# Optimization experiments

Hardware: AMD Instinct MI355X
Metric: run time of the kernel (lower is better)

## Reference

```python
import jax, jax.numpy as jnp
import numpy as np

B, N, DIM = 1, 65536, 256
H, D, G = 8, 64, 64  # heads, dim_head, slice_num


def setup_inputs() -> dict:
    key = jax.random.key(0)
    ks = jax.random.split(key, 16)
    s = 0.02
    return {
        "x": jax.random.normal(ks[0], (B, N, DIM), jnp.float32),
        "Wx": jax.random.normal(ks[1], (H * D, DIM), jnp.float32) * s,
        "bx": jnp.zeros((H * D,), jnp.float32),
        "Wt1": jax.random.normal(ks[2], (G, D), jnp.float32) * s,
        "bt1": jnp.zeros((G,), jnp.float32),
        "Wt2": jax.random.normal(ks[3], (1, G), jnp.float32) * s,
        "bt2": jnp.zeros((1,), jnp.float32),
        "bias": jnp.ones((1, H, 1, 1), jnp.float32) * 0.5,
        "Ws": jax.random.normal(ks[4], (G, D), jnp.float32) * s,
        "bs": jnp.zeros((G,), jnp.float32),
        "Wq": jax.random.normal(ks[5], (D, D), jnp.float32) * s,
        "Wk": jax.random.normal(ks[6], (D, D), jnp.float32) * s,
        "Wv": jax.random.normal(ks[7], (D, D), jnp.float32) * s,
        "Wout": jax.random.normal(ks[8], (DIM, H * D), jnp.float32) * s,
        "bout": jnp.zeros((DIM,), jnp.float32),
        "u": jax.random.uniform(ks[9], (B, H, N, G), jnp.float32),
    }


def _gelu(t):
    return jax.nn.gelu(t, approximate=False)  # torch default exact GELU


def reference(x, Wx, bx, Wt1, bt1, Wt2, bt2, bias, Ws, bs, Wq, Wk, Wv, Wout, bout, u):
    b, n, _ = x.shape
    h, d, g = Wt1.shape[1] and bias.shape[1], Wq.shape[0], Ws.shape[0]
    # project and split heads: b n (h d) -> b h n d
    x_mid = (x @ Wx.T + bx).reshape(b, n, h, d).transpose(0, 2, 1, 3)
    # per-point temperature MLP + learned bias, clamped
    temp = _gelu(_gelu(x_mid @ Wt1.T + bt1) @ Wt2.T + bt2) + bias  # (b,h,n,1)
    temp = jnp.maximum(temp, 0.01)
    # gumbel-softmax slice routing (soft, hard=False)
    logits = x_mid @ Ws.T + bs  # (b,h,n,g)
    gnoise = -jnp.log(-jnp.log(u + 1e-8) + 1e-8)
    slice_weights = jax.nn.softmax((logits + gnoise) / temp, axis=-1)
    norm = slice_weights.sum(axis=2)  # (b,h,g)
    # gather-aggregate points into g slice tokens
    slice_tokens = jnp.einsum('bhnc,bhng->bhgc', x_mid, slice_weights)
    slice_tokens = slice_tokens / (norm[..., None] + 1e-5)
    # tiny g x g attention among slice tokens
    q = slice_tokens @ Wq.T
    k = slice_tokens @ Wk.T
    v = slice_tokens @ Wv.T
    attn = jax.nn.softmax((q @ k.transpose(0, 1, 3, 2)) * (d ** -0.5), axis=-1)
    out_slice = attn @ v  # (b,h,g,d)
    # scatter-combine back to points
    out = jnp.einsum('bhgd,bhng->bhnd', out_slice, slice_weights)
    out = out.transpose(0, 2, 1, 3).reshape(b, n, h * d)
    return out @ Wout.T + bout
```

## Files before the change

### kernel.cpp

```cpp
#include <hip/hip_runtime.h>
#include <math.h>

#define NPTS  65536
#define DIMX  256
#define NH    8
#define HDIM  512

typedef __attribute__((ext_vector_type(4))) float f32x4;
typedef __attribute__((ext_vector_type(8))) short short8;
typedef __attribute__((ext_vector_type(8))) unsigned short ushort8;
typedef __attribute__((ext_vector_type(4))) unsigned short us4;

__device__ __forceinline__ ushort f2bf(float f) {
    unsigned x = __float_as_uint(f);
    return (ushort)((x + 0x7fffu + ((x >> 16) & 1u)) >> 16);
}
__device__ __forceinline__ float bf2f(ushort u) {
    return __uint_as_float((unsigned)u << 16);
}
__device__ __forceinline__ float erf_fast(float x) {
    float ax = fabsf(x);
    float t  = __builtin_amdgcn_rcpf(1.0f + 0.3275911f * ax);
    float p  = fmaf(fmaf(fmaf(fmaf(1.061405429f, t, -1.453152027f), t,
                   1.421413741f), t, -0.284496736f), t, 0.254829592f) * t;
    float y  = 1.0f - p * __expf(-ax * ax);
    return copysignf(y, x);
}
__device__ __forceinline__ float gelu_fast(float x) {
    return 0.5f * x * (1.0f + erf_fast(x * 0.7071067811865476f));
}

__global__ __launch_bounds__(256)
void prep_kernel(const float* __restrict__ x, const float* __restrict__ Wx,
                 const float* __restrict__ Ws, const float* __restrict__ Wt1,
                 ushort* __restrict__ xb, ushort* __restrict__ Wxb,
                 ushort* __restrict__ wb) {
    const int t = threadIdx.x;
    const int b = blockIdx.x;
    if (b < 8192) {
        size_t idx = (size_t)b * 2048 + t * 8;
        float4 a0 = *(const float4*)&x[idx];
        float4 a1 = *(const float4*)&x[idx + 4];
        ushort8 v = { f2bf(a0.x), f2bf(a0.y), f2bf(a0.z), f2bf(a0.w),
                      f2bf(a1.x), f2bf(a1.y), f2bf(a1.z), f2bf(a1.w) };
        *(ushort8*)&xb[idx] = v;
    } else if (b < 8256) {
        int idx = (b - 8192) * 2048 + t * 8;
        float4 a0 = *(const float4*)&Wx[idx];
        float4 a1 = *(const float4*)&Wx[idx + 4];
        ushort8 v = { f2bf(a0.x), f2bf(a0.y), f2bf(a0.z), f2bf(a0.w),
                      f2bf(a1.x), f2bf(a1.y), f2bf(a1.z), f2bf(a1.w) };
        *(ushort8*)&Wxb[idx] = v;
    } else {
        int idx = (b - 8256) * 2048 + t * 8;
        int row = idx >> 6, col = idx & 63;
        const float* src = (row < 64) ? &Ws[row * 64 + col]
                                      : &Wt1[(row - 64) * 64 + col];
        float4 a0 = *(const float4*)src;
        float4 a1 = *(const float4*)(src + 4);
        ushort8 v = { f2bf(a0.x), f2bf(a0.y), f2bf(a0.z), f2bf(a0.w),
                      f2bf(a1.x), f2bf(a1.y), f2bf(a1.z), f2bf(a1.w) };
        *(ushort8*)&wb[idx] = v;
    }
}

__global__ __launch_bounds__(256)
void xmid_lgt1_kernel(const ushort* __restrict__ A, const ushort* __restrict__ B,
                      const float* __restrict__ bias,
                      const ushort* __restrict__ wb,
                      const float* __restrict__ bs,  const float* __restrict__ bt1,
                      const float* __restrict__ Wt2, const float* __restrict__ bt2,
                      const float* __restrict__ biasp,
                      const float* __restrict__ u,
                      ushort* __restrict__ xmb, ushort* __restrict__ swb) {
    __shared__ __align__(16) ushort pool[2][128][64];
    const int hp = blockIdx.y;
    const int m0 = blockIdx.x * 128, n0 = hp * 128;
    const int t = threadIdx.x, l = t & 63, w = t >> 6;
    const int wr = w >> 1, wc = w & 1;
    const int lr = l & 15, lq = l >> 4;
    const float LOG2E = 1.4426950408889634f;
    const float LN2   = 0.6931471805599453f;
    const float SH2   = 36.0673760222f;

    f32x4 acc[4][4];
    #pragma unroll
    for (int mi = 0; mi < 4; ++mi)
        #pragma unroll
        for (int ni = 0; ni < 4; ++ni) acc[mi][ni] = (f32x4){0.f, 0.f, 0.f, 0.f};

    for (int ks = 0; ks < 4; ++ks) {
        __syncthreads();
        #pragma unroll
        for (int i = 0; i < 4; ++i) {
            int idx = i * 256 + t;
            int row = idx >> 3, g = idx & 7;
            ushort8 av = *(const ushort8*)&A[(size_t)(m0 + row) * 256 + ks * 64 + g * 8];
            *(ushort8*)&pool[0][row][(g ^ (row & 7)) * 8] = av;
            ushort8 bv = *(const ushort8*)&B[(size_t)(n0 + row) * 256 + ks * 64 + g * 8];
            *(ushort8*)&pool[1][row][(g ^ (row & 7)) * 8] = bv;
        }
        __syncthreads();
        #pragma unroll
        for (int kf = 0; kf < 2; ++kf) {
            short8 af[4], bfr[4];
            #pragma unroll
            for (int mi = 0; mi < 4; ++mi) {
                int row = wr * 64 + mi * 16 + lr, g = kf * 4 + lq;
                af[mi] = *(const short8*)&pool[0][row][(g ^ (row & 7)) * 8];
            }
            #pragma unroll
            for (int ni = 0; ni < 4; ++ni) {
                int row = wc * 64 + ni * 16 + lr, g = kf * 4 + lq;
                bfr[ni] = *(const short8*)&pool[1][row][(g ^ (row & 7)) * 8];
            }
            #pragma unroll
            for (int mi = 0; mi < 4; ++mi)
                #pragma unroll
                for (int ni = 0; ni < 4; ++ni)
                    acc[mi][ni] = __builtin_amdgcn_mfma_f32_16x16x32_bf16(
                        af[mi], bfr[ni], acc[mi][ni], 0, 0, 0);
        }
    }

    __syncthreads();
    ushort (* __restrict__ Xl)[128] = (ushort (*)[128])(&pool[0][0][0]);
    #pragma unroll
    for (int ni = 0; ni < 4; ++ni) {
        int colL = wc * 64 + ni * 16 + lr;
        float bb = bias[n0 + colL];
        int gg = colL >> 3, c7 = colL & 7;
        #pragma unroll
        for (int mi = 0; mi < 4; ++mi)
            #pragma unroll
            for (int j = 0; j < 4; ++j) {
                int row = wr * 64 + mi * 16 + lq * 4 + j;
                Xl[row][(gg ^ (row & 7)) * 8 + c7] = f2bf(acc[mi][ni][j] + bb);
            }
    }
    __syncthreads();
    #pragma unroll
    for (int i = 0; i < 8; ++i) {
        int e = i * 256 + t;
        int row = e >> 4, gg = e & 15;
        ushort8 v = *(const ushort8*)&Xl[row][(gg ^ (row & 7)) * 8];
        *(ushort8*)&xmb[(size_t)(m0 + row) * 512 + n0 + gg * 8] = v;
    }

    const float bt2v = bt2[0];
    float bsr[4], bt1r[4], wt2r[4];
    #pragma unroll
    for (int ni = 0; ni < 4; ++ni) {
        bsr[ni]  = bs [ni * 16 + lr];
        bt1r[ni] = bt1[ni * 16 + lr];
        wt2r[ni] = Wt2[ni * 16 + lr];
    }

    #pragma unroll
    for (int hh = 0; hh < 2; ++hh) {
        const int h = hp * 2 + hh;
        const float biasph = biasp[h];

        f32x4 acc2[2][8];
        #pragma unroll
        for (int mi = 0; mi < 2; ++mi)
            #pragma unroll
            for (int ni = 0; ni < 8; ++ni) acc2[mi][ni] = (f32x4){0.f, 0.f, 0.f, 0.f};

        #pragma unroll
        for (int kf = 0; kf < 2; ++kf) {
            const int g = kf * 4 + lq;
            short8 af[2], bfr[8];
            #pragma unroll
            for (int mi = 0; mi < 2; ++mi) {
                int row = w * 32 + mi * 16 + lr;
                int gg = hh * 8 + g;
                af[mi] = *(const short8*)&Xl[row][(gg ^ (row & 7)) * 8];
            }
            #pragma unroll
            for (int ni = 0; ni < 8; ++ni)
                bfr[ni] = *(const short8*)&wb[(size_t)(ni * 16 + lr) * 64 + g * 8];
            #pragma unroll
            for (int mi = 0; mi < 2; ++mi)
                #pragma unroll
                for (int ni = 0; ni < 8; ++ni)
                    acc2[mi][ni] = __builtin_amdgcn_mfma_f32_16x16x32_bf16(
                        af[mi], bfr[ni], acc2[mi][ni], 0, 0, 0);
        }

        #pragma unroll
        for (int mi = 0; mi < 2; ++mi) {
            float uu[4][4];
            #pragma unroll
            for (int jj = 0; jj < 4; ++jj) {
                const int n = m0 + w * 32 + mi * 16 + lq * 4 + jj;
                const float* up = &u[((size_t)h * NPTS + n) * 64 + lr];
                #pragma unroll
                for (int ni = 0; ni < 4; ++ni) uu[jj][ni] = up[ni * 16];
            }
            float ts[4];
            #pragma unroll
            for (int jj = 0; jj < 4; ++jj) {
                float s = 0.f;
                #pragma unroll
                for (int ni = 0; ni < 4; ++ni)
                    s += gelu_fast(acc2[mi][ni + 4][jj] + bt1r[ni]) * wt2r[ni];
                ts[jj] = s;
            }
            #pragma unroll
            for (int off = 1; off <= 8; off <<= 1) {
                #pragma unroll
                for (int jj = 0; jj < 4; ++jj) ts[jj] += __shfl_xor(ts[jj], off);
            }
            float invt[4], invt2[4];
            #pragma unroll
            for (int jj = 0; jj < 4; ++jj) {
                float tmp = gelu_fast(ts[jj] + bt2v) + biasph;
                tmp = fmaxf(tmp, 0.01f);
                invt[jj]  = __builtin_amdgcn_rcpf(tmp);
                invt2[jj] = invt[jj] * LOG2E;
            }
            float sv[4][4], ps[4] = {0.f, 0.f, 0.f, 0.f};
            #pragma unroll
            for (int jj = 0; jj < 4; ++jj) {
                #pragma unroll
                for (int ni = 0; ni < 4; ++ni) {
                    float L1 = __log2f(uu[jj][ni] + 1e-8f);
                    float inner = fmaf(-LN2, L1, 1e-8f);
                    float L2v = __log2f(inner);
                    float base = fmaf(acc2[mi][ni][jj] + bsr[ni], invt2[jj], -SH2);
                    sv[jj][ni] = __builtin_amdgcn_exp2f(fmaf(-invt[jj], L2v, base));
                    ps[jj] += sv[jj][ni];
                }
            }
            #pragma unroll
            for (int off = 1; off <= 8; off <<= 1) {
                #pragma unroll
                for (int jj = 0; jj < 4; ++jj) ps[jj] += __shfl_xor(ps[jj], off);
            }
            #pragma unroll
            for (int jj = 0; jj < 4; ++jj) {
                const int n = m0 + w * 32 + mi * 16 + lq * 4 + jj;
                const float inv = __builtin_amdgcn_rcpf(ps[jj]);
                ushort* sp = &swb[(size_t)n * 512 + h * 64 + lr];
                #pragma unroll
                for (int ni = 0; ni < 4; ++ni)
                    sp[ni * 16] = f2bf(sv[jj][ni] * inv);
            }
        }
    }
}

__global__ __launch_bounds__(256)
void gather_mfma_kernel(const ushort* __restrict__ xmb, const ushort* __restrict__ swb,
                        float* __restrict__ stp, float* __restrict__ normp) {
    __shared__ __align__(16) ushort tile[2][64][128];
    ushort (* __restrict__ swT)[128] = tile[0];
    ushort (* __restrict__ xT )[128] = tile[1];
    const int h  = blockIdx.y;
    const int n0 = blockIdx.x * 1024;
    const int t  = threadIdx.x, l = t & 63, w = t >> 6;
    const int lr = l & 15, lq = l >> 4;
    const int gb = t & 7;
    const int ng = t >> 3;

    f32x4 acc[4][4];
    #pragma unroll
    for (int gi = 0; gi < 4; ++gi)
        #pragma unroll
        for (int ci = 0; ci < 4; ++ci) acc[gi][ci] = (f32x4){0.f, 0.f, 0.f, 0.f};
    float nrm8[8];
    #pragma unroll
    for (int j = 0; j < 8; ++j) nrm8[j] = 0.f;

    for (int r = 0; r < 8; ++r) {
        const int nt = n0 + r * 128;
        ushort8 sv[4], xv[4];
        #pragma unroll
        for (int i = 0; i < 4; ++i) {
            int n = nt + ng * 4 + i;
            sv[i] = *(const ushort8*)&swb[(size_t)n * 512 + h * 64 + gb * 8];
            xv[i] = *(const ushort8*)&xmb[(size_t)n * 512 + h * 64 + gb * 8];
        }
        __syncthreads();
        #pragma unroll
        for (int j = 0; j < 8; ++j) {
            int g   = gb * 8 + j;
            int swz = (ng >> 1) ^ (g & 7) ^ ((g >> 3) & 7);
            int off = swz * 8 + (ng & 1) * 4;
            us4 s4 = { sv[0][j], sv[1][j], sv[2][j], sv[3][j] };
            us4 x4 = { xv[0][j], xv[1][j], xv[2][j], xv[3][j] };
            *(us4*)&swT[g][off] = s4;
            *(us4*)&xT [g][off] = x4;
            nrm8[j] += (bf2f(sv[0][j]) + bf2f(sv[1][j]))
                     + (bf2f(sv[2][j]) + bf2f(sv[3][j]));
        }
        __syncthreads();
        short8 af[4], bfr[4];
        #pragma unroll
        for (int gi = 0; gi < 4; ++gi) {
            int g   = gi * 16 + lr;
            int swz = (w * 4 + lq) ^ (g & 7) ^ ((g >> 3) & 7);
            af[gi]  = *(const short8*)&swT[g][swz * 8];
            bfr[gi] = *(const short8*)&xT [g][swz * 8];
        }
        #pragma unroll
        for (int gi = 0; gi < 4; ++gi)
            #pragma unroll
            for (int ci = 0; ci < 4; ++ci)
                acc[gi][ci] = __builtin_amdgcn_mfma_f32_16x16x32_bf16(
                    af[gi], bfr[ci], acc[gi][ci], 0, 0, 0);
    }

    float* sred = (float*)tile;
    const size_t stbase = ((size_t)h * 64 + blockIdx.x) * 4096;
    #pragma unroll
    for (int half = 0; half < 2; ++half) {
        __syncthreads();
        #pragma unroll
        for (int gg = 0; gg < 2; ++gg) {
            int gi = half * 2 + gg;
            #pragma unroll
            for (int ci = 0; ci < 4; ++ci)
                #pragma unroll
                for (int j = 0; j < 4; ++j)
                    sred[(w * 32 + gg * 16 + lq * 4 + j) * 64 + ci * 16 + lr]
                        = acc[gi][ci][j];
        }
        __syncthreads();
        #pragma unroll
        for (int i = 0; i < 8; ++i) {
            int e = i * 256 + t;
            float s = (sred[e] + sred[2048 + e]) + (sred[4096 + e] + sred[6144 + e]);
            stp[stbase + half * 2048 + e] = s;
        }
    }

    __syncthreads();
    float* narr = (float*)tile;
    #pragma unroll
    for (int j = 0; j < 8; ++j) narr[ng * 64 + gb * 8 + j] = nrm8[j];
    __syncthreads();
    if (t < 64) {
        float s = 0.f;
        #pragma unroll 8
        for (int k = 0; k < 32; ++k) s += narr[k * 64 + t];
        normp[((size_t)h * 64 + blockIdx.x) * 64 + t] = s;
    }
}

__global__ __launch_bounds__(256)
void reduce_st_kernel(const float* __restrict__ stp, const float* __restrict__ normp,
                      float* __restrict__ st_red, float* __restrict__ nrm) {
    const int h = blockIdx.x;
    const int e = blockIdx.y * 256 + threadIdx.x;
    float s = 0.f;
    #pragma unroll 8
    for (int ch = 0; ch < 64; ++ch)
        s += stp[((size_t)h * 64 + ch) * 4096 + e];
    st_red[(size_t)h * 4096 + e] = s;
    if (blockIdx.y == 0 && threadIdx.x < 64) {
        float ns = 0.f;
        #pragma unroll 8
        for (int ch = 0; ch < 64; ++ch)
            ns += normp[((size_t)h * 64 + ch) * 64 + threadIdx.x];
        nrm[h * 64 + threadIdx.x] = ns + 1e-5f;
    }
}

__global__ __launch_bounds__(256)
void attn_small_kernel(const float* __restrict__ st_red, const float* __restrict__ nrm,
                       const float* __restrict__ Wq, const float* __restrict__ Wk,
                       const float* __restrict__ Wv, float* __restrict__ osl) {
    __shared__ float st[64][68];
    __shared__ float ql[64][68];
    __shared__ float kl[64][68];
    __shared__ float vl[64][68];
    __shared__ float sc[64][68];
    __shared__ float nl[64];
    const int h = blockIdx.x;
    const int t = threadIdx.x;

    if (t < 64) nl[t] = nrm[h * 64 + t];
    __syncthreads();
    for (int e = t; e < 4096; e += 256)
        st[e>>6][e&63] = st_red[(size_t)h * 4096 + e] / nl[e>>6];
    __syncthreads();
    for (int e = t; e < 4096; e += 256) {
        int g = e >> 6, dd = e & 63;
        float aq = 0.f, ak = 0.f, av = 0.f;
        for (int cc = 0; cc < 64; ++cc) {
            float sv = st[g][cc];
            aq = fmaf(sv, Wq[dd*64 + cc], aq);
            ak = fmaf(sv, Wk[dd*64 + cc], ak);
            av = fmaf(sv, Wv[dd*64 + cc], av);
        }
        ql[g][dd] = aq; kl[g][dd] = ak; vl[g][dd] = av;
    }
    __syncthreads();
    for (int e = t; e < 4096; e += 256) {
        int g = e >> 6, gp = e & 63;
        float s = 0.f;
        for (int dd = 0; dd < 64; ++dd) s = fmaf(ql[g][dd], kl[gp][dd], s);
        sc[g][gp] = s * 0.125f;
    }
    __syncthreads();
    if (t < 64) {
        float m = -1e30f;
        for (int j = 0; j < 64; ++j) m = fmaxf(m, sc[t][j]);
        float ssum = 0.f;
        for (int j = 0; j < 64; ++j) { float p = expf(sc[t][j] - m); sc[t][j] = p; ssum += p; }
        float inv = 1.f / ssum;
        for (int j = 0; j < 64; ++j) sc[t][j] *= inv;
    }
    __syncthreads();
    for (int e = t; e < 4096; e += 256) {
        int g = e >> 6, dd = e & 63;
        float s = 0.f;
        for (int gp = 0; gp < 64; ++gp) s = fmaf(sc[g][gp], vl[gp][dd], s);
        osl[(size_t)h * 4096 + e] = s;
    }
}

__global__ __launch_bounds__(256)
void fold_kernel(const float* __restrict__ osl, const float* __restrict__ Wout,
                 ushort* __restrict__ Mtb) {
    __shared__ float os[64][65];
    __shared__ float wl[128][65];
    const int h  = blockIdx.x;
    const int i0 = blockIdx.y * 128;
    const int t  = threadIdx.x;
    for (int e = t; e < 4096; e += 256) os[e>>6][e&63] = osl[(size_t)h * 4096 + e];
    for (int e = t; e < 8192; e += 256) {
        int i = e >> 6, d = e & 63;
        wl[i][d] = Wout[(size_t)(i0 + i) * HDIM + h * 64 + d];
    }
    __syncthreads();
    const int g = t & 63, iq = t >> 6;
    #pragma unroll 4
    for (int k = 0; k < 32; ++k) {
        int i = iq * 32 + k;
        float s = 0.f;
        #pragma unroll
        for (int d = 0; d < 64; ++d) s = fmaf(os[g][d], wl[i][d], s);
        Mtb[(size_t)(i0 + i) * HDIM + h * 64 + g] = f2bf(s);
    }
}

__global__ __launch_bounds__(256)
void gemm_out_kernel(const ushort* __restrict__ A, const ushort* __restrict__ B,
                     const float* __restrict__ bias, float* __restrict__ C) {
    __shared__ __align__(16) ushort Al[128][64];
    __shared__ __align__(16) ushort Bl[128][64];
    const int m0 = blockIdx.x * 128, n0 = blockIdx.y * 128;
    const int t = threadIdx.x, l = t & 63, w = t >> 6;
    const int wr = w >> 1, wc = w & 1;
    const int lr = l & 15, lq = l >> 4;

    f32x4 acc[4][4];
    #pragma unroll
    for (int mi = 0; mi < 4; ++mi)
        #pragma unroll
        for (int ni = 0; ni < 4; ++ni) acc[mi][ni] = (f32x4){0.f, 0.f, 0.f, 0.f};

    for (int ks = 0; ks < 8; ++ks) {
        __syncthreads();
        #pragma unroll
        for (int i = 0; i < 4; ++i) {
            int idx = i * 256 + t;
            int row = idx >> 3, g = idx & 7;
            ushort8 av = *(const ushort8*)&A[(size_t)(m0 + row) * 512 + ks * 64 + g * 8];
            *(ushort8*)&Al[row][(g ^ (row & 7)) * 8] = av;
            ushort8 bv = *(const ushort8*)&B[(size_t)(n0 + row) * 512 + ks * 64 + g * 8];
            *(ushort8*)&Bl[row][(g ^ (row & 7)) * 8] = bv;
        }
        __syncthreads();
        #pragma unroll
        for (int kf = 0; kf < 2; ++kf) {
            short8 af[4], bfr[4];
            #pragma unroll
            for (int mi = 0; mi < 4; ++mi) {
                int row = wr * 64 + mi * 16 + lr, g = kf * 4 + lq;
                af[mi] = *(const short8*)&Al[row][(g ^ (row & 7)) * 8];
            }
            #pragma unroll
            for (int ni = 0; ni < 4; ++ni) {
                int row = wc * 64 + ni * 16 + lr, g = kf * 4 + lq;
                bfr[ni] = *(const short8*)&Bl[row][(g ^ (row & 7)) * 8];
            }
            #pragma unroll
            for (int mi = 0; mi < 4; ++mi)
                #pragma unroll
                for (int ni = 0; ni < 4; ++ni)
                    acc[mi][ni] = __builtin_amdgcn_mfma_f32_16x16x32_bf16(
                        af[mi], bfr[ni], acc[mi][ni], 0, 0, 0);
        }
    }
    #pragma unroll
    for (int ni = 0; ni < 4; ++ni) {
        int col = n0 + wc * 64 + ni * 16 + lr;
        float bb = bias[col];
        #pragma unroll
        for (int mi = 0; mi < 4; ++mi)
            #pragma unroll
            for (int j = 0; j < 4; ++j) {
                int row = m0 + wr * 64 + mi * 16 + lq * 4 + j;
                C[(size_t)row * 256 + col] = acc[mi][ni][j] + bb;
            }
    }
}

extern "C" void kernel_launch(void* const* d_in, const int* in_sizes, int n_in,
                              void* d_out, int out_size, void* d_ws, size_t ws_size,
                              hipStream_t stream) {
    const float* x    = (const float*)d_in[0];
    const float* Wx   = (const float*)d_in[1];
    const float* bx   = (const float*)d_in[2];
    const float* Wt1  = (const float*)d_in[3];
    const float* bt1  = (const float*)d_in[4];
    const float* Wt2  = (const float*)d_in[5];
    const float* bt2  = (const float*)d_in[6];
    const float* biasp= (const float*)d_in[7];
    const float* Ws   = (const float*)d_in[8];
    const float* bs   = (const float*)d_in[9];
    const float* Wq   = (const float*)d_in[10];
    const float* Wk   = (const float*)d_in[11];
    const float* Wv   = (const float*)d_in[12];
    const float* Wout = (const float*)d_in[13];
    const float* bout = (const float*)d_in[14];
    const float* u    = (const float*)d_in[15];
    float* out = (float*)d_out;

    float*  stp    = (float*)d_ws;
    float*  normp  = stp    + (size_t)NH * 64 * 4096;
    float*  st_red = normp  + (size_t)NH * 64 * 64;
    float*  nrm    = st_red + (size_t)NH * 4096;
    float*  osl    = nrm    + (size_t)NH * 64;
    ushort* wb     = (ushort*)(osl + (size_t)NH * 4096);
    ushort* Wxb    = wb  + (size_t)128 * 64;
    ushort* Mtb    = Wxb + (size_t)HDIM * DIMX;
    ushort* xb     = Mtb + (size_t)DIMX * HDIM;
    ushort* xmb    = xb  + (size_t)NPTS * DIMX;
    ushort* swb    = xmb + (size_t)NPTS * HDIM;

    prep_kernel<<<8260, 256, 0, stream>>>(x, Wx, Ws, Wt1, xb, Wxb, wb);
    xmid_lgt1_kernel<<<dim3(512, 4), 256, 0, stream>>>(xb, Wxb, bx, wb, bs, bt1,
                                                       Wt2, bt2, biasp, u,
                                                       xmb, swb);
    gather_mfma_kernel<<<dim3(64, 8), 256, 0, stream>>>(xmb, swb, stp, normp);
    reduce_st_kernel<<<dim3(8, 16), 256, 0, stream>>>(stp, normp, st_red, nrm);
    attn_small_kernel<<<8, 256, 0, stream>>>(st_red, nrm, Wq, Wk, Wv, osl);
    fold_kernel<<<dim3(8, 2), 256, 0, stream>>>(osl, Wout, Mtb);
    gemm_out_kernel<<<dim3(512, 2), 256, 0, stream>>>(swb, Mtb, bout, out);
}
```

Measured before the change: 259.4 us.

## Fuse small attention with output-weight fold and loop both N-halves per GEMM block

The tiny per-head attention kernel now also folds its output through Wout directly from shared memory, removing one kernel launch and the osl round-trip. The output GEMM launches 512 blocks that each compute both 128-column halves sequentially, so the A tile is read by one block instead of two. The fold now runs on only 8 blocks instead of 16, which lengthens that serial step, and the GEMM grid is halved, which lowers parallelism across CUs.

```diff
diff --git a/kernel.cpp b/kernel.cpp
--- a/kernel.cpp
+++ b/kernel.cpp
@@ -369,15 +369,17 @@
 }
 
 __global__ __launch_bounds__(256)
-void attn_small_kernel(const float* __restrict__ st_red, const float* __restrict__ nrm,
-                       const float* __restrict__ Wq, const float* __restrict__ Wk,
-                       const float* __restrict__ Wv, float* __restrict__ osl) {
+void attn_fold_kernel(const float* __restrict__ st_red, const float* __restrict__ nrm,
+                      const float* __restrict__ Wq, const float* __restrict__ Wk,
+                      const float* __restrict__ Wv, const float* __restrict__ Wout,
+                      ushort* __restrict__ Mtb) {
     __shared__ float st[64][68];
     __shared__ float ql[64][68];
     __shared__ float kl[64][68];
     __shared__ float vl[64][68];
     __shared__ float sc[64][68];
     __shared__ float nl[64];
+    __shared__ float wl[128][65];
     const int h = blockIdx.x;
     const int t = threadIdx.x;
 
@@ -418,32 +420,27 @@
         int g = e >> 6, dd = e & 63;
         float s = 0.f;
         for (int gp = 0; gp < 64; ++gp) s = fmaf(sc[g][gp], vl[gp][dd], s);
-        osl[(size_t)h * 4096 + e] = s;
-    }
-}
-
-__global__ __launch_bounds__(256)
-void fold_kernel(const float* __restrict__ osl, const float* __restrict__ Wout,
-                 ushort* __restrict__ Mtb) {
-    __shared__ float os[64][65];
-    __shared__ float wl[128][65];
-    const int h  = blockIdx.x;
-    const int i0 = blockIdx.y * 128;
-    const int t  = threadIdx.x;
-    for (int e = t; e < 4096; e += 256) os[e>>6][e&63] = osl[(size_t)h * 4096 + e];
-    for (int e = t; e < 8192; e += 256) {
-        int i = e >> 6, d = e & 63;
-        wl[i][d] = Wout[(size_t)(i0 + i) * HDIM + h * 64 + d];
+        st[g][dd] = s;
     }
     __syncthreads();
     const int g = t & 63, iq = t >> 6;
-    #pragma unroll 4
-    for (int k = 0; k < 32; ++k) {
-        int i = iq * 32 + k;
-        float s = 0.f;
-        #pragma unroll
-        for (int d = 0; d < 64; ++d) s = fmaf(os[g][d], wl[i][d], s);
-        Mtb[(size_t)(i0 + i) * HDIM + h * 64 + g] = f2bf(s);
+    #pragma unroll
+    for (int half = 0; half < 2; ++half) {
+        const int i0 = half * 128;
+        for (int e = t; e < 8192; e += 256) {
+            int i = e >> 6, d = e & 63;
+            wl[i][d] = Wout[(size_t)(i0 + i) * HDIM + h * 64 + d];
+        }
+        __syncthreads();
+        #pragma unroll 4
+        for (int k = 0; k < 32; ++k) {
+            int i = iq * 32 + k;
+            float s = 0.f;
+            #pragma unroll
+            for (int d = 0; d < 64; ++d) s = fmaf(st[g][d], wl[i][d], s);
+            Mtb[(size_t)(i0 + i) * HDIM + h * 64 + g] = f2bf(s);
+        }
+        __syncthreads();
     }
 }
 
@@ -452,61 +449,65 @@
                      const float* __restrict__ bias, float* __restrict__ C) {
     __shared__ __align__(16) ushort Al[128][64];
     __shared__ __align__(16) ushort Bl[128][64];
-    const int m0 = blockIdx.x * 128, n0 = blockIdx.y * 128;
+    const int m0 = blockIdx.x * 128;
     const int t = threadIdx.x, l = t & 63, w = t >> 6;
     const int wr = w >> 1, wc = w & 1;
     const int lr = l & 15, lq = l >> 4;
 
-    f32x4 acc[4][4];
-    #pragma unroll
-    for (int mi = 0; mi < 4; ++mi)
-        #pragma unroll
-        for (int ni = 0; ni < 4; ++ni) acc[mi][ni] = (f32x4){0.f, 0.f, 0.f, 0.f};
-
-    for (int ks = 0; ks < 8; ++ks) {
-        __syncthreads();
-        #pragma unroll
-        for (int i = 0; i < 4; ++i) {
-            int idx = i * 256 + t;
-            int row = idx >> 3, g = idx & 7;
-            ushort8 av = *(const ushort8*)&A[(size_t)(m0 + row) * 512 + ks * 64 + g * 8];
-            *(ushort8*)&Al[row][(g ^ (row & 7)) * 8] = av;
-            ushort8 bv = *(const ushort8*)&B[(size_t)(n0 + row) * 512 + ks * 64 + g * 8];
-            *(ushort8*)&Bl[row][(g ^ (row & 7)) * 8] = bv;
-        }
-        __syncthreads();
-        #pragma unroll
-        for (int kf = 0; kf < 2; ++kf) {
-            short8 af[4], bfr[4];
-            #pragma unroll
-            for (int mi = 0; mi < 4; ++mi) {
-                int row = wr * 64 + mi * 16 + lr, g = kf * 4 + lq;
-                af[mi] = *(const short8*)&Al[row][(g ^ (row & 7)) * 8];
-            }
-            #pragma unroll
-            for (int ni = 0; ni < 4; ++ni) {
-                int row = wc * 64 + ni * 16 + lr, g = kf * 4 + lq;
-                bfr[ni] = *(const short8*)&Bl[row][(g ^ (row & 7)) * 8];
-            }
+    #pragma unroll 1
+    for (int p = 0; p < 2; ++p) {
+        const int n0 = p * 128;
+        f32x4 acc[4][4];
+        #pragma unroll
+        for (int mi = 0; mi < 4; ++mi)
+            #pragma unroll
+            for (int ni = 0; ni < 4; ++ni) acc[mi][ni] = (f32x4){0.f, 0.f, 0.f, 0.f};
+
+        for (int ks = 0; ks < 8; ++ks) {
+            __syncthreads();
+            #pragma unroll
+            for (int i = 0; i < 4; ++i) {
+                int idx = i * 256 + t;
+                int row = idx >> 3, g = idx & 7;
+                ushort8 av = *(const ushort8*)&A[(size_t)(m0 + row) * 512 + ks * 64 + g * 8];
+                *(ushort8*)&Al[row][(g ^ (row & 7)) * 8] = av;
+                ushort8 bv = *(const ushort8*)&B[(size_t)(n0 + row) * 512 + ks * 64 + g * 8];
+                *(ushort8*)&Bl[row][(g ^ (row & 7)) * 8] = bv;
+            }
+            __syncthreads();
+            #pragma unroll
+            for (int kf = 0; kf < 2; ++kf) {
+                short8 af[4], bfr[4];
+                #pragma unroll
+                for (int mi = 0; mi < 4; ++mi) {
+                    int row = wr * 64 + mi * 16 + lr, g = kf * 4 + lq;
+                    af[mi] = *(const short8*)&Al[row][(g ^ (row & 7)) * 8];
+                }
+                #pragma unroll
+                for (int ni = 0; ni < 4; ++ni) {
+                    int row = wc * 64 + ni * 16 + lr, g = kf * 4 + lq;
+                    bfr[ni] = *(const short8*)&Bl[row][(g ^ (row & 7)) * 8];
+                }
+                #pragma unroll
+                for (int mi = 0; mi < 4; ++mi)
+                    #pragma unroll
+                    for (int ni = 0; ni < 4; ++ni)
+                        acc[mi][ni] = __builtin_amdgcn_mfma_f32_16x16x32_bf16(
+                            af[mi], bfr[ni], acc[mi][ni], 0, 0, 0);
+            }
+        }
+        #pragma unroll
+        for (int ni = 0; ni < 4; ++ni) {
+            int col = n0 + wc * 64 + ni * 16 + lr;
+            float bb = bias[col];
             #pragma unroll
             for (int mi = 0; mi < 4; ++mi)
                 #pragma unroll
-                for (int ni = 0; ni < 4; ++ni)
-                    acc[mi][ni] = __builtin_amdgcn_mfma_f32_16x16x32_bf16(
-                        af[mi], bfr[ni], acc[mi][ni], 0, 0, 0);
-        }
-    }
-    #pragma unroll
-    for (int ni = 0; ni < 4; ++ni) {
-        int col = n0 + wc * 64 + ni * 16 + lr;
-        float bb = bias[col];
-        #pragma unroll
-        for (int mi = 0; mi < 4; ++mi)
-            #pragma unroll
-            for (int j = 0; j < 4; ++j) {
-                int row = m0 + wr * 64 + mi * 16 + lq * 4 + j;
-                C[(size_t)row * 256 + col] = acc[mi][ni][j] + bb;
-            }
+                for (int j = 0; j < 4; ++j) {
+                    int row = m0 + wr * 64 + mi * 16 + lq * 4 + j;
+                    C[(size_t)row * 256 + col] = acc[mi][ni][j] + bb;
+                }
+        }
     }
 }
 
@@ -549,7 +550,6 @@
                                                        xmb, swb);
     gather_mfma_kernel<<<dim3(64, 8), 256, 0, stream>>>(xmb, swb, stp, normp);
     reduce_st_kernel<<<dim3(8, 16), 256, 0, stream>>>(stp, normp, st_red, nrm);
-    attn_small_kernel<<<8, 256, 0, stream>>>(st_red, nrm, Wq, Wk, Wv, osl);
-    fold_kernel<<<dim3(8, 2), 256, 0, stream>>>(osl, Wout, Mtb);
-    gemm_out_kernel<<<dim3(512, 2), 256, 0, stream>>>(swb, Mtb, bout, out);
-}
+    attn_fold_kernel<<<8, 256, 0, stream>>>(st_red, nrm, Wq, Wk, Wv, Wout, Mtb);
+    gemm_out_kernel<<<dim3(512), 256, 0, stream>>>(swb, Mtb, bout, out);
+}
```

Measured after the change: 288.1 us. 11.1% more time.
